# Kernel optimization log

Hardware: AMD Instinct MI355X
Metric: run time of the kernel (lower is better)

Reference implementation:

```python
import jax, jax.numpy as jnp
import numpy as np

B = 64      # num graphs
NPG = 800   # nodes per graph
N = B * NPG
EPG = 6400  # edges per graph (avg degree 8)
APG = 64    # feasible actions per graph
H = 4       # attention heads
C = 64      # hidden channels per head
OUT = 128   # out_channels


def _gat_params(key, fin, h, c, concat):
    k1, k2, k3 = jax.random.split(key, 3)
    s = 1.0 / np.sqrt(fin)
    W = jax.random.uniform(k1, (fin, h * c), jnp.float32, -s, s)
    a_src = jax.random.uniform(k2, (h, c), jnp.float32, -s, s)
    a_dst = jax.random.uniform(k3, (h, c), jnp.float32, -s, s)
    b = jnp.zeros((h * c if concat else c,), jnp.float32)
    return W, a_src, a_dst, b


def _lin_params(key, fin, fout):
    k1, k2 = jax.random.split(key)
    s = 1.0 / np.sqrt(fin)
    W = jax.random.uniform(k1, (fin, fout), jnp.float32, -s, s)
    b = jax.random.uniform(k2, (fout,), jnp.float32, -s, s)
    return W, b


def setup_inputs() -> dict:
    key = jax.random.key(0)
    ks = list(jax.random.split(key, 24))
    x = jax.random.normal(ks[0], (N, 5), jnp.float32)
    offs = jnp.arange(B, dtype=jnp.int32) * NPG
    src = jax.random.randint(ks[1], (B, EPG), 0, NPG, jnp.int32) + offs[:, None]
    dst = jax.random.randint(ks[2], (B, EPG), 0, NPG, jnp.int32) + offs[:, None]
    edge_index = jnp.stack([src.reshape(-1), dst.reshape(-1)])
    batch = jnp.repeat(jnp.arange(B, dtype=jnp.int32), NPG)
    actions_idx = (jax.random.randint(ks[3], (B, APG, 2), 0, NPG, jnp.int32)
                   + offs[:, None, None]).reshape(-1, 2)
    tabu_label = (jax.random.uniform(ks[4], (B * APG, 1)) < 0.5).astype(jnp.float32)
    inp = dict(x=x, edge_index=edge_index, batch=batch,
               actions_idx=actions_idx, tabu_label=tabu_label)
    names = ['f1', 'f2', 'f3', 'b1', 'b2', 'b3']
    fins = [3, H * C, H * C, 3, H * C, H * C]
    hs = [H, H, 1, H, H, 1]
    cs = [C, C, OUT, C, C, OUT]
    concats = [True, True, False, True, True, False]
    for i, nm in enumerate(names):
        W, a_s, a_d, b = _gat_params(ks[5 + i], fins[i], hs[i], cs[i], concats[i])
        inp[nm + '_W'] = W; inp[nm + '_as'] = a_s; inp[nm + '_ad'] = a_d; inp[nm + '_b'] = b
    dims = [(8 * OUT + 1, 2 * OUT), (2 * OUT, 2 * OUT), (2 * OUT, 2 * OUT), (2 * OUT, 1)]
    for i, (fi, fo) in enumerate(dims):
        W, b = _lin_params(ks[12 + i], fi, fo)
        inp['p_W%d' % (i + 1)] = W; inp['p_b%d' % (i + 1)] = b
    return inp


def _gat(h, s, d, W, a_src, a_dst, bias, concat):
    # PyG GATConv: project, per-edge attention, softmax over target index, scatter-add
    n = h.shape[0]
    Hh, Cc = a_src.shape
    xp = (h @ W).reshape(n, Hh, Cc)                      # [N,H,C]
    al_s = (xp * a_src).sum(-1)                          # [N,H]
    al_d = (xp * a_dst).sum(-1)                          # [N,H]
    e = jax.nn.leaky_relu(al_s[s] + al_d[d], 0.2)        # [E,H]
    m = jax.ops.segment_max(e, d, num_segments=n)
    ex = jnp.exp(e - m[d])
    den = jax.ops.segment_sum(ex, d, num_segments=n)
    alpha = ex / (den[d] + 1e-16)
    out = jax.ops.segment_sum(xp[s] * alpha[..., None], d, num_segments=n)  # [N,H,C]
    out = out.reshape(n, Hh * Cc) if concat else out.mean(axis=1)
    return out + bias


def reference(x, edge_index, batch, actions_idx, tabu_label,
              f1_W, f1_as, f1_ad, f1_b, f2_W, f2_as, f2_ad, f2_b,
              f3_W, f3_as, f3_ad, f3_b, b1_W, b1_as, b1_ad, b1_b,
              b2_W, b2_as, b2_ad, b2_b, b3_W, b3_as, b3_ad, b3_b,
              p_W1, p_b1, p_W2, p_b2, p_W3, p_b3, p_W4, p_b4):
    n = x.shape[0]
    ar = jnp.arange(n, dtype=edge_index.dtype)
    ei = jnp.concatenate([edge_index, jnp.stack([ar, ar])], axis=1)  # add_self_loops
    src, dst = ei[0], ei[1]
    # forward branch (flow source_to_target)
    hf = x[:, jnp.array([0, 1, 3])]
    hf = jax.nn.elu(_gat(hf, src, dst, f1_W, f1_as, f1_ad, f1_b, True))
    hf = jax.nn.elu(_gat(hf, src, dst, f2_W, f2_as, f2_ad, f2_b, True))
    hf3 = _gat(hf, src, dst, f3_W, f3_as, f3_ad, f3_b, False)
    # backward branch (flow target_to_source == reversed edges)
    hb = x[:, jnp.array([0, 2, 4])]
    hb = jax.nn.elu(_gat(hb, dst, src, b1_W, b1_as, b1_ad, b1_b, True))
    hb = jax.nn.elu(_gat(hb, dst, src, b2_W, b2_as, b2_ad, b2_b, True))
    hb3 = _gat(hb, dst, src, b3_W, b3_as, b3_ad, b3_b, False)
    h_node = jnp.concatenate([hf3, hb3], axis=-1)        # [N, 2*OUT]
    counts = jax.ops.segment_sum(jnp.ones((n,), x.dtype), batch, num_segments=B)
    g_pool = jax.ops.segment_sum(h_node, batch, num_segments=B) / counts[:, None]
    node_h = jnp.concatenate([h_node, g_pool[batch]], axis=-1)  # [N, 4*OUT]
    action_h = jnp.concatenate([node_h[actions_idx[:, 0]],
                                node_h[actions_idx[:, 1]],
                                tabu_label], axis=-1)    # [A, 8*OUT+1]
    h = jnp.tanh(action_h @ p_W1 + p_b1)
    h = jnp.tanh(h @ p_W2 + p_b2)
    h = jnp.tanh(h @ p_W3 + p_b3)
    score = (h @ p_W4 + p_b4).reshape(B, APG)
    log_prob = jax.nn.log_softmax(score, axis=-1)        # [B, APG]
    entropy = -(jnp.exp(log_prob) * log_prob).sum(-1, keepdims=True)  # [B,1]
    return (log_prob, entropy)
```

## Files before the change

### kernel.cpp

```cpp
#include <hip/hip_runtime.h>
#include <hip/hip_bf16.h>
#include <math.h>

constexpr int NN  = 51200;
constexpr int EE  = 409600;
constexpr int BB  = 64;
constexpr int APG = 64;
constexpr int NPG = 800;
constexpr int SCAN_N = 2 * NN;
constexpr int NA = BB * APG;
constexpr int KF = 1056;

typedef __bf16 bf16x8 __attribute__((ext_vector_type(8)));
typedef float f32x4 __attribute__((ext_vector_type(4)));
typedef float f32x2 __attribute__((ext_vector_type(2)));
typedef __attribute__((address_space(1))) const void g_void;
typedef __attribute__((address_space(3))) void l_void;

__device__ __forceinline__ float leaky(float x) { return x > 0.f ? x : 0.2f * x; }
__device__ __forceinline__ float bflo(unsigned w) { return __uint_as_float(w << 16); }
__device__ __forceinline__ float bfhi(unsigned w) { return __uint_as_float(w & 0xffff0000u); }
__device__ __forceinline__ unsigned short f2b(float x) {
  __hip_bfloat16 h = __float2bfloat16(x);
  unsigned short u;
  __builtin_memcpy(&u, &h, 2);
  return u;
}
__device__ __forceinline__ unsigned pack2(float a, float b) {
  return (unsigned)f2b(a) | ((unsigned)f2b(b) << 16);
}

__global__ void count_kernel(const int* __restrict__ ei, int* cnt) {
  int e = blockIdx.x * blockDim.x + threadIdx.x;
  if (e >= EE) return;
  int s = ei[e], d = ei[EE + e];
  atomicAdd(&cnt[d], 1);
  atomicAdd(&cnt[NN + s], 1);
}

__global__ __launch_bounds__(256) void scan1_kernel(const int* __restrict__ cnt,
                                                    int* __restrict__ rp,
                                                    int* __restrict__ bsum) {
  __shared__ int wsum[4];
  int b = blockIdx.x, t = threadIdx.x;
  int base = b * 1024 + t * 4;
  int4 v = *(const int4*)(cnt + base);
  int s = v.x + v.y + v.z + v.w;
  int lane = t & 63, wv = t >> 6;
  int incl = s;
  for (int off = 1; off < 64; off <<= 1) {
    int u = __shfl_up(incl, off);
    if (lane >= off) incl += u;
  }
  if (lane == 63) wsum[wv] = incl;
  __syncthreads();
  int woff = 0;
  for (int i = 0; i < wv; i++) woff += wsum[i];
  int excl = woff + incl - s;
  rp[base] = excl;
  rp[base + 1] = excl + v.x;
  rp[base + 2] = excl + v.x + v.y;
  rp[base + 3] = excl + v.x + v.y + v.z;
  if (t == 255) bsum[b] = woff + incl;
}

__global__ void scan2_kernel(const int* __restrict__ bsum, int* __restrict__ boff,
                             int* __restrict__ rp) {
  __shared__ int w0;
  int t = threadIdx.x;
  int v = (t < 100) ? bsum[t] : 0;
  int lane = t & 63;
  int incl = v;
  for (int off = 1; off < 64; off <<= 1) {
    int u = __shfl_up(incl, off);
    if (lane >= off) incl += u;
  }
  if (t == 63) w0 = incl;
  __syncthreads();
  int excl = incl - v + ((t >= 64) ? w0 : 0);
  if (t < 100) boff[t] = excl;
  if (t == 99) rp[SCAN_N] = excl + v;
}

__global__ __launch_bounds__(256) void scan3_kernel(int* __restrict__ rp,
                                                    const int* __restrict__ boff) {
  int b = blockIdx.x;
  int off = boff[b];
  int i = b * 1024 + threadIdx.x * 4;
  int4 v = *(int4*)(rp + i);
  v.x += off; v.y += off; v.z += off; v.w += off;
  *(int4*)(rp + i) = v;
}

__global__ void fill_kernel(const int* __restrict__ ei, const int* __restrict__ rp,
                            int* pos, int* __restrict__ col) {
  int e = blockIdx.x * blockDim.x + threadIdx.x;
  if (e >= EE) return;
  int s = ei[e], d = ei[EE + e];
  int p = atomicAdd(&pos[d], 1);
  col[rp[d] + p] = s;
  int q = atomicAdd(&pos[NN + s], 1);
  col[rp[NN + s] + q] = d;
}

__global__ __launch_bounds__(256) void precomp_kernel(const float* __restrict__ Wf,
                                                      const float* __restrict__ Wb,
                                                      const float* __restrict__ asf,
                                                      const float* __restrict__ adf,
                                                      const float* __restrict__ asb,
                                                      const float* __restrict__ adb,
                                                      float* __restrict__ wa) {
  int wave = (blockIdx.x * blockDim.x + threadIdx.x) >> 6;
  int lane = threadIdx.x & 63;
  if (wave >= 48) return;
  int dir = wave / 24, sd = (wave / 12) % 2, h = (wave / 3) % 4, c = wave % 3;
  const float* W = dir ? Wb : Wf;
  const float* a = dir ? (sd ? adb : asb) : (sd ? adf : asf);
  float v = W[c * 256 + h * 64 + lane] * a[h * 64 + lane];
  for (int off = 1; off < 64; off <<= 1) v += __shfl_xor(v, off);
  if (lane == 0) wa[wave] = v;
}

__global__ __launch_bounds__(256) void lin1_kernel(const float* __restrict__ x,
                                                   const float* __restrict__ Wf,
                                                   const float* __restrict__ Wb,
                                                   __hip_bfloat16* __restrict__ out) {
  int idx = blockIdx.x * 256 + threadIdx.x;
  int n = idx >> 5, grp = idx & 31;
  int dir = (n >= NN) ? 1 : 0;
  int node = dir ? n - NN : n;
  const float* W = dir ? Wb : Wf;
  int c1 = dir ? 2 : 1, c2 = dir ? 4 : 3;
  float f0 = x[node * 5], f1 = x[node * 5 + c1], f2 = x[node * 5 + c2];
  int j0 = grp * 8;
  float v[8];
#pragma unroll
  for (int j = 0; j < 8; j++)
    v[j] = f0 * W[j0 + j] + f1 * W[256 + j0 + j] + f2 * W[512 + j0 + j];
  uint4 u;
  u.x = pack2(v[0], v[1]);
  u.y = pack2(v[2], v[3]);
  u.z = pack2(v[4], v[5]);
  u.w = pack2(v[6], v[7]);
  *(uint4*)(out + (size_t)n * 256 + j0) = u;
}

__global__ __launch_bounds__(256) void al1_kernel(const float* __restrict__ x,
                                                  const float* __restrict__ wa,
                                                  float* __restrict__ al_s,
                                                  float* __restrict__ al_d) {
  int idx = blockIdx.x * 256 + threadIdx.x;
  int n = idx >> 2, h = idx & 3;
  int dir = (n >= NN) ? 1 : 0;
  int node = dir ? n - NN : n;
  int c1 = dir ? 2 : 1, c2 = dir ? 4 : 3;
  float f0 = x[node * 5], f1 = x[node * 5 + c1], f2 = x[node * 5 + c2];
  const float* ws = wa + dir * 24 + h * 3;
  const float* wd = wa + dir * 24 + 12 + h * 3;
  al_s[idx] = f0 * ws[0] + f1 * ws[1] + f2 * ws[2];
  al_d[idx] = f0 * wd[0] + f1 * wd[1] + f2 * wd[2];
}

template <int HH>
__global__ __launch_bounds__(256) void alpha_kernel(const float* __restrict__ als,
                                                    const float* __restrict__ ald,
                                                    const int* __restrict__ rp,
                                                    const int* __restrict__ col,
                                                    float* __restrict__ alpha,
                                                    float* __restrict__ alpha_self) {
  int b = blockIdx.x;
  int xcd = b & 7, q = b >> 3;
  int g2 = (q / 25) * 8 + xcd;
  int d = g2 * 800 + (q % 25) * 32 + (threadIdx.x >> 3);
  int slot = threadIdx.x & 7;
  int off_row = (d >= NN) ? NN : 0;
  float ald_loc[HH], self_lg[HH];
#pragma unroll
  for (int h = 0; h < HH; h++) {
    ald_loc[h] = ald[d * HH + h];
    self_lg[h] = leaky(als[d * HH + h] + ald_loc[h]);
  }
  int beg = rp[d], end = rp[d + 1];
  int i0 = beg + slot;
  bool have = i0 < end;
  int s0 = col[have ? i0 : beg] + off_row;
  float mx[HH], lg0[HH];
#pragma unroll
  for (int h = 0; h < HH; h++) mx[h] = self_lg[h];
  if (have) {
#pragma unroll
    for (int h = 0; h < HH; h++) {
      lg0[h] = leaky(als[s0 * HH + h] + ald_loc[h]);
      mx[h] = fmaxf(mx[h], lg0[h]);
    }
  }
  for (int i = i0 + 8; i < end; i += 8) {
    int s = col[i] + off_row;
#pragma unroll
    for (int h = 0; h < HH; h++) mx[h] = fmaxf(mx[h], leaky(als[s * HH + h] + ald_loc[h]));
  }
#pragma unroll
  for (int h = 0; h < HH; h++) {
    mx[h] = fmaxf(mx[h], __shfl_xor(mx[h], 1));
    mx[h] = fmaxf(mx[h], __shfl_xor(mx[h], 2));
    mx[h] = fmaxf(mx[h], __shfl_xor(mx[h], 4));
  }
  float sm[HH], w0[HH];
#pragma unroll
  for (int h = 0; h < HH; h++) sm[h] = 0.f;
  if (have) {
#pragma unroll
    for (int h = 0; h < HH; h++) {
      w0[h] = __expf(lg0[h] - mx[h]);
      sm[h] += w0[h];
    }
  }
  for (int i = i0 + 8; i < end; i += 8) {
    int s = col[i] + off_row;
#pragma unroll
    for (int h = 0; h < HH; h++) {
      float w = __expf(leaky(als[s * HH + h] + ald_loc[h]) - mx[h]);
      sm[h] += w;
      alpha[(size_t)i * HH + h] = w;
    }
  }
#pragma unroll
  for (int h = 0; h < HH; h++) {
    sm[h] += __shfl_xor(sm[h], 1);
    sm[h] += __shfl_xor(sm[h], 2);
    sm[h] += __shfl_xor(sm[h], 4);
  }
  float inv[HH];
#pragma unroll
  for (int h = 0; h < HH; h++)
    inv[h] = 1.f / (sm[h] + __expf(self_lg[h] - mx[h]) + 1e-16f);
  if (have) {
#pragma unroll
    for (int h = 0; h < HH; h++) alpha[(size_t)i0 * HH + h] = w0[h] * inv[h];
  }
  for (int i = i0 + 8; i < end; i += 8)
#pragma unroll
    for (int h = 0; h < HH; h++) alpha[(size_t)i * HH + h] *= inv[h];
  if (slot == 0) {
#pragma unroll
    for (int h = 0; h < HH; h++)
      alpha_self[d * HH + h] = __expf(self_lg[h] - mx[h]) * inv[h];
  }
}

template <int ND>
__device__ __forceinline__ void load_dw(const unsigned* p, unsigned* w) {
  if constexpr (ND == 4) {
    uint4 v = *(const uint4*)p;
    w[0] = v.x; w[1] = v.y; w[2] = v.z; w[3] = v.w;
  } else {
    uint2 v = *(const uint2*)p;
    w[0] = v.x; w[1] = v.y;
  }
}
__device__ __forceinline__ f32x2 unpk(unsigned w) {
  f32x2 v;
  v.x = bflo(w);
  v.y = bfhi(w);
  return v;
}

template <int HH, int CC, int OUT_SPLIT>
__global__ __launch_bounds__(256) void spmm_kernel(const __hip_bfloat16* __restrict__ xp,
                                                   const float* __restrict__ alpha,
                                                   const float* __restrict__ alpha_self,
                                                   const int* __restrict__ rp,
                                                   const int* __restrict__ col,
                                                   const float* __restrict__ biasf,
                                                   const float* __restrict__ biasb,
                                                   __hip_bfloat16* __restrict__ out_bf,
                                                   int do_elu) {
  constexpr int HC = HH * CC;
  constexpr int CPL = HC / 32;
  constexpr int NW = CPL / 2;
  int b = blockIdx.x;
  int xcd = b & 7, q = b >> 3;
  int g2 = (q / 200) * 8 + xcd;
  int d = g2 * 800 + (q % 200) * 4 + (threadIdx.x >> 6);
  int off_row = (d >= NN) ? NN : 0;
  const float* bias = (d >= NN) ? biasb : biasf;
  int lane = threadIdx.x & 63;
  int sub = lane & 31, g = lane >> 5;
  int h_l = (sub * CPL) / CC;
  const unsigned* xw = (const unsigned*)xp;
  size_t rowoff = (size_t)sub * NW;
  f32x2 acc[NW];
#pragma unroll
  for (int j = 0; j < NW; j++) acc[j] = (f32x2)(0.f);
  int beg = rp[d], end = rp[d + 1];
  int deg = end - beg;
  if (g == 0) {
    float a = alpha_self[d * HH + h_l];
    unsigned w[NW];
    load_dw<NW>(xw + (size_t)d * (HC / 2) + rowoff, w);
#pragma unroll
    for (int q2 = 0; q2 < NW; q2++) acc[q2] += a * unpk(w[q2]);
  }
  for (int it = 0; it * 4 < deg; it++) {
    int e1 = beg + it * 4 + g;
    int e2 = e1 + 2;
    bool p1 = e1 < end, p2 = e2 < end;
    int ec1 = p1 ? e1 : beg, ec2 = p2 ? e2 : beg;
    int s1 = col[ec1] + off_row, s2 = col[ec2] + off_row;
    float a1 = p1 ? alpha[(size_t)ec1 * HH + h_l] : 0.f;
    float a2 = p2 ? alpha[(size_t)ec2 * HH + h_l] : 0.f;
    unsigned w1[NW], w2[NW];
    load_dw<NW>(xw + (size_t)s1 * (HC / 2) + rowoff, w1);
    load_dw<NW>(xw + (size_t)s2 * (HC / 2) + rowoff, w2);
#pragma unroll
    for (int q2 = 0; q2 < NW; q2++)
      acc[q2] += a1 * unpk(w1[q2]) + a2 * unpk(w2[q2]);
  }
#pragma unroll
  for (int j = 0; j < NW; j++) {
    acc[j].x += __shfl_xor(acc[j].x, 32);
    acc[j].y += __shfl_xor(acc[j].y, 32);
  }
  if (g == 0) {
    float v[CPL];
#pragma unroll
    for (int j = 0; j < NW; j++) {
      v[2 * j] = acc[j].x + bias[sub * CPL + 2 * j];
      v[2 * j + 1] = acc[j].y + bias[sub * CPL + 2 * j + 1];
    }
    if (do_elu) {
#pragma unroll
      for (int j = 0; j < CPL; j++) v[j] = v[j] > 0.f ? v[j] : (__expf(v[j]) - 1.f);
    }
    unsigned* ob;
    if constexpr (OUT_SPLIT) {
      int nd = (d < NN) ? d : d - NN;
      int oo = (d < NN) ? 0 : 64;
      ob = (unsigned*)out_bf + (size_t)nd * 128 + oo + sub * NW;
    } else {
      ob = (unsigned*)out_bf + (size_t)d * (HC / 2) + rowoff;
    }
#pragma unroll
    for (int q2 = 0; q2 < NW; q2++)
      ob[q2] = pack2(v[2 * q2], v[2 * q2 + 1]);
  }
}

__global__ void castW2_kernel(const float* __restrict__ W0, const float* __restrict__ W1,
                              __hip_bfloat16* __restrict__ Wt0,
                              __hip_bfloat16* __restrict__ Wt1,
                              int K, int N, int Kp) {
  int idx = blockIdx.x * 256 + threadIdx.x;
  int tot = N * Kp;
  if (idx >= 2 * tot) return;
  const float* W = (idx < tot) ? W0 : W1;
  __hip_bfloat16* Wt = (idx < tot) ? Wt0 : Wt1;
  int i = (idx < tot) ? idx : idx - tot;
  int n = i / Kp, k = i % Kp;
  Wt[i] = (k < K) ? __float2bfloat16(W[(size_t)k * N + n]) : __float2bfloat16(0.f);
}

template <int EPI, int ALH, int ALCC>
__global__ __launch_bounds__(256) void gemm_mfma(const __hip_bfloat16* __restrict__ A,
                                                 const __hip_bfloat16* __restrict__ Bt0,
                                                 const __hip_bfloat16* __restrict__ Bt1,
                                                 __hip_bfloat16* __restrict__ Cb,
                                                 const float* __restrict__ bias0,
                                                 const float* __restrict__ bias1,
                                                 const float* __restrict__ asv0,
                                                 const float* __restrict__ asv1,
                                                 const float* __restrict__ adv0,
                                                 const float* __restrict__ adv1,
                                                 float* __restrict__ al_s,
                                                 float* __restrict__ al_d,
                                                 int M, int N, int K, int Mhalf) {
  __shared__ __align__(16) __hip_bfloat16 As[128 * 32];
  __shared__ __align__(16) __hip_bfloat16 Bs[128 * 32];
  int t = threadIdx.x;
  int wave = t >> 6, lane = t & 63;
  int wm = (wave >> 1) * 64, wn = (wave & 1) * 64;
  int bm = blockIdx.y * 128, bn = blockIdx.x * 128;
  bool second = bm >= Mhalf;
  const __hip_bfloat16* Bt = second ? Bt1 : Bt0;
  const float* bias = second ? bias1 : bias0;
  const float* asv = second ? asv1 : asv0;
  const float* adv = second ? adv1 : adv0;

  int r0 = t >> 2, c0 = (t & 3) * 8;
  const __hip_bfloat16* Ag0 = A + (size_t)(bm + r0) * K + c0;
  const __hip_bfloat16* Ag1 = A + (size_t)(bm + r0 + 64) * K + c0;
  const __hip_bfloat16* Bg0 = Bt + (size_t)(bn + r0) * K + c0;
  const __hip_bfloat16* Bg1 = Bt + (size_t)(bn + r0 + 64) * K + c0;
  __hip_bfloat16* Asp0 = As + t * 8;
  __hip_bfloat16* Asp1 = As + 64 * 8 * 4 + t * 8;
  __hip_bfloat16* Bsp0 = Bs + t * 8;
  __hip_bfloat16* Bsp1 = Bs + 64 * 8 * 4 + t * 8;

  f32x4 acc[4][4];
#pragma unroll
  for (int i = 0; i < 4; i++)
#pragma unroll
    for (int j = 0; j < 4; j++) acc[i][j] = (f32x4)(0.f);

  int frag_off = (lane & 15) * 32 + (lane >> 4) * 8;
  const __hip_bfloat16* Ab = As + wm * 32 + frag_off;
  const __hip_bfloat16* Bb = Bs + wn * 32 + frag_off;

  for (int k0 = 0; k0 < K; k0 += 32) {
    __syncthreads();
    __builtin_amdgcn_global_load_lds((g_void*)(Ag0 + k0), (l_void*)Asp0, 16, 0, 0);
    __builtin_amdgcn_global_load_lds((g_void*)(Ag1 + k0), (l_void*)Asp1, 16, 0, 0);
    __builtin_amdgcn_global_load_lds((g_void*)(Bg0 + k0), (l_void*)Bsp0, 16, 0, 0);
    __builtin_amdgcn_global_load_lds((g_void*)(Bg1 + k0), (l_void*)Bsp1, 16, 0, 0);
    __syncthreads();
    bf16x8 af[4], bfr[4];
#pragma unroll
    for (int i = 0; i < 4; i++) af[i] = *(const bf16x8*)(Ab + i * 16 * 32);
#pragma unroll
    for (int j = 0; j < 4; j++) bfr[j] = *(const bf16x8*)(Bb + j * 16 * 32);
#pragma unroll
    for (int i = 0; i < 4; i++)
#pragma unroll
      for (int j = 0; j < 4; j++)
        acc[i][j] = __builtin_amdgcn_mfma_f32_16x16x32_bf16(af[i], bfr[j], acc[i][j], 0, 0, 0);
  }

  int cr = (lane >> 4) * 4, cc = lane & 15;

  if constexpr (ALH > 0) {
    int head = (bn + wn) / ALCC;
    float as_c[4], ad_c[4];
#pragma unroll
    for (int j = 0; j < 4; j++) {
      int colx = bn + wn + j * 16 + cc;
      as_c[j] = asv[colx];
      ad_c[j] = adv[colx];
    }
#pragma unroll
    for (int i = 0; i < 4; i++)
#pragma unroll
      for (int r = 0; r < 4; r++) {
        float ps = 0.f, pd = 0.f;
#pragma unroll
        for (int j = 0; j < 4; j++) {
          ps += acc[i][j][r] * as_c[j];
          pd += acc[i][j][r] * ad_c[j];
        }
        ps += __shfl_xor(ps, 1); pd += __shfl_xor(pd, 1);
        ps += __shfl_xor(ps, 2); pd += __shfl_xor(pd, 2);
        ps += __shfl_xor(ps, 4); pd += __shfl_xor(pd, 4);
        ps += __shfl_xor(ps, 8); pd += __shfl_xor(pd, 8);
        if ((lane & 15) == 0) {
          int row = bm + wm + i * 16 + cr + r;
          if (ALCC > 64) {
            atomicAdd(&al_s[row * ALH + head], ps);
            atomicAdd(&al_d[row * ALH + head], pd);
          } else {
            al_s[row * ALH + head] = ps;
            al_d[row * ALH + head] = pd;
          }
        }
      }
  }

#pragma unroll
  for (int i = 0; i < 4; i++)
#pragma unroll
    for (int j = 0; j < 4; j++) {
      int colx = bn + wn + j * 16 + cc;
      float bs = (EPI == 2) ? bias[colx] : 0.f;
#pragma unroll
      for (int r = 0; r < 4; r++) {
        float v = acc[i][j][r];
        if (EPI == 2) v = tanhf(v + bs);
        Cb[(size_t)(bm + wm + i * 16 + cr + r) * N + colx] = __float2bfloat16(v);
      }
    }
}

__global__ void pool1_kernel(const __hip_bfloat16* __restrict__ h_node,
                             float* __restrict__ part) {
  int g = blockIdx.y, c = blockIdx.x, t = threadIdx.x;
  const unsigned* base = (const unsigned*)h_node + ((size_t)g * NPG + c * 100) * 128 + t;
  f32x2 s = (f32x2)(0.f);
  for (int i = 0; i < 100; i++) {
    unsigned w = base[(size_t)i * 128];
    s += unpk(w);
  }
  part[(size_t)(g * 8 + c) * 256 + 2 * t] = s.x;
  part[(size_t)(g * 8 + c) * 256 + 2 * t + 1] = s.y;
}

__global__ void pool2_kernel(const float* __restrict__ part, float* __restrict__ g_pool) {
  int g = blockIdx.x, t = threadIdx.x;
  float s = 0.f;
  for (int c = 0; c < 8; c++) s += part[(size_t)(g * 8 + c) * 256 + t];
  g_pool[g * 256 + t] = s * (1.f / NPG);
}

__global__ __launch_bounds__(256) void buildfeat_kernel(const __hip_bfloat16* __restrict__ h_node,
                                                        const float* __restrict__ g_pool,
                                                        const int* __restrict__ actions,
                                                        const float* __restrict__ tabu,
                                                        const int* __restrict__ batch,
                                                        __hip_bfloat16* __restrict__ feat) {
  int a = (blockIdx.x * blockDim.x + threadIdx.x) >> 6;
  int lane = threadIdx.x & 63;
  if (a >= NA) return;
  int n0 = actions[a * 2], n1 = actions[a * 2 + 1];
  int g = batch[n0];
  ushort4 v0 = *(const ushort4*)(h_node + (size_t)n0 * 256 + lane * 4);
  float4 vg = *(const float4*)(g_pool + (size_t)g * 256 + lane * 4);
  ushort4 v1 = *(const ushort4*)(h_node + (size_t)n1 * 256 + lane * 4);
  __hip_bfloat16* fr = feat + (size_t)a * KF;
  ushort4 ug = make_ushort4(f2b(vg.x), f2b(vg.y), f2b(vg.z), f2b(vg.w));
  *(ushort4*)(fr + lane * 4) = v0;
  *(ushort4*)(fr + 256 + lane * 4) = ug;
  *(ushort4*)(fr + 512 + lane * 4) = v1;
  *(ushort4*)(fr + 768 + lane * 4) = ug;
  if (lane < 8) {
    float t0 = (lane == 0) ? tabu[a] : 0.f;
    ushort4 u = make_ushort4(f2b(t0), 0, 0, 0);
    *(ushort4*)(fr + 1024 + lane * 4) = u;
  }
}

__global__ __launch_bounds__(256) void gemv_kernel(const __hip_bfloat16* __restrict__ y,
                                                   const float* __restrict__ W4,
                                                   const float* __restrict__ b4,
                                                   float* __restrict__ scores) {
  int a = (blockIdx.x * blockDim.x + threadIdx.x) >> 6;
  int lane = threadIdx.x & 63;
  if (a >= NA) return;
  const unsigned* row = (const unsigned*)(y + (size_t)a * 256);
  float s = 0.f;
#pragma unroll
  for (int q = 0; q < 2; q++) {
    unsigned w = row[lane * 2 + q];
    s += bflo(w) * W4[lane * 4 + 2 * q] + bfhi(w) * W4[lane * 4 + 2 * q + 1];
  }
  for (int off = 1; off < 64; off <<= 1) s += __shfl_xor(s, off);
  if (lane == 0) scores[a] = s + b4[0];
}

__global__ void softmax_kernel(const float* __restrict__ scores, float* __restrict__ out) {
  int g = (blockIdx.x * blockDim.x + threadIdx.x) >> 6;
  int lane = threadIdx.x & 63;
  if (g >= BB) return;
  float s = scores[g * 64 + lane];
  float m = s;
  for (int off = 1; off < 64; off <<= 1) m = fmaxf(m, __shfl_xor(m, off));
  float ex = expf(s - m);
  float sum = ex;
  for (int off = 1; off < 64; off <<= 1) sum += __shfl_xor(sum, off);
  float lp = s - m - logf(sum);
  out[g * 64 + lane] = lp;
  float pe = (ex / sum) * lp;
  for (int off = 1; off < 64; off <<= 1) pe += __shfl_xor(pe, off);
  if (lane == 0) out[BB * APG + g] = -pe;
}

extern "C" void kernel_launch(void* const* d_in, const int* in_sizes, int n_in,
                              void* d_out, int out_size, void* d_ws, size_t ws_size,
                              hipStream_t stream) {
  const float* x = (const float*)d_in[0];
  const int* ei = (const int*)d_in[1];
  const int* batch = (const int*)d_in[2];
  const int* actions = (const int*)d_in[3];
  const float* tabu = (const float*)d_in[4];
  const float* fW[3] = {(const float*)d_in[5], (const float*)d_in[9], (const float*)d_in[13]};
  const float* fas[3] = {(const float*)d_in[6], (const float*)d_in[10], (const float*)d_in[14]};
  const float* fad[3] = {(const float*)d_in[7], (const float*)d_in[11], (const float*)d_in[15]};
  const float* fb[3] = {(const float*)d_in[8], (const float*)d_in[12], (const float*)d_in[16]};
  const float* bW[3] = {(const float*)d_in[17], (const float*)d_in[21], (const float*)d_in[25]};
  const float* bas[3] = {(const float*)d_in[18], (const float*)d_in[22], (const float*)d_in[26]};
  const float* bad[3] = {(const float*)d_in[19], (const float*)d_in[23], (const float*)d_in[27]};
  const float* bb[3] = {(const float*)d_in[20], (const float*)d_in[24], (const float*)d_in[28]};
  const float* pW1 = (const float*)d_in[29];
  const float* pb1 = (const float*)d_in[30];
  const float* pW2 = (const float*)d_in[31];
  const float* pb2 = (const float*)d_in[32];
  const float* pW3 = (const float*)d_in[33];
  const float* pb3 = (const float*)d_in[34];
  const float* pW4 = (const float*)d_in[35];
  const float* pb4 = (const float*)d_in[36];
  float* out = (float*)d_out;

  char* ws = (char*)d_ws;
  size_t o = 0;
  auto alloc = [&](size_t bytes) -> void* {
    o = (o + 255) & ~(size_t)255;
    void* p = ws + o;
    o += bytes;
    return p;
  };
  int* cnt = (int*)alloc((size_t)4 * NN * 4);
  int* rp = (int*)alloc((size_t)(SCAN_N + 1) * 4);
  int* col = (int*)alloc(((size_t)2 * EE + 64) * 4);
  int* bsum = (int*)alloc(128 * 4);
  int* boff = (int*)alloc(128 * 4);
  float* al_s = (float*)alloc((size_t)SCAN_N * 4 * 4);
  float* al_d = (float*)alloc((size_t)SCAN_N * 4 * 4);
  float* alpha = (float*)alloc((size_t)2 * EE * 4 * 4);
  float* alpha_self = (float*)alloc((size_t)SCAN_N * 4 * 4);
  float* wa = (float*)alloc(64 * 4);
  __hip_bfloat16* xp = (__hip_bfloat16*)alloc((size_t)SCAN_N * 256 * 2);
  __hip_bfloat16* bufA = (__hip_bfloat16*)alloc((size_t)SCAN_N * 256 * 2);
  __hip_bfloat16* h_node = (__hip_bfloat16*)alloc((size_t)NN * 256 * 2);
  __hip_bfloat16* wt0 = (__hip_bfloat16*)alloc((size_t)256 * KF * 2);
  __hip_bfloat16* wt1 = (__hip_bfloat16*)alloc((size_t)256 * KF * 2);
  float* part = (float*)alloc((size_t)BB * 8 * 256 * 4);
  float* g_pool = (float*)alloc((size_t)BB * 256 * 4);
  float* scores = (float*)alloc((size_t)NA * 4);
  __hip_bfloat16* feat = xp;
  __hip_bfloat16* y1 = feat + (size_t)NA * KF;
  __hip_bfloat16* y2 = y1 + (size_t)NA * 256;

  hipMemsetAsync(cnt, 0, (size_t)4 * NN * 4, stream);
  count_kernel<<<(EE + 255) / 256, 256, 0, stream>>>(ei, cnt);
  scan1_kernel<<<SCAN_N / 1024, 256, 0, stream>>>(cnt, rp, bsum);
  scan2_kernel<<<1, 128, 0, stream>>>(bsum, boff, rp);
  scan3_kernel<<<SCAN_N / 1024, 256, 0, stream>>>(rp, boff);
  fill_kernel<<<(EE + 255) / 256, 256, 0, stream>>>(ei, rp, cnt + 2 * NN, col);

  const int nwb = SCAN_N / 4;
  const int nab = SCAN_N * 8 / 256;

  precomp_kernel<<<12, 256, 0, stream>>>(fW[0], bW[0], fas[0], fad[0], bas[0], bad[0], wa);
  lin1_kernel<<<SCAN_N * 32 / 256, 256, 0, stream>>>(x, fW[0], bW[0], xp);
  al1_kernel<<<SCAN_N * 4 / 256, 256, 0, stream>>>(x, wa, al_s, al_d);
  alpha_kernel<4><<<nab, 256, 0, stream>>>(al_s, al_d, rp, col, alpha, alpha_self);
  spmm_kernel<4, 64, 0><<<nwb, 256, 0, stream>>>(xp, alpha, alpha_self, rp, col,
                                                 fb[0], bb[0], bufA, 1);
  castW2_kernel<<<(2 * 256 * 256 + 255) / 256, 256, 0, stream>>>(fW[1], bW[1], wt0, wt1,
                                                                 256, 256, 256);
  gemm_mfma<1, 4, 64><<<dim3(2, SCAN_N / 128), 256, 0, stream>>>(
      bufA, wt0, wt1, xp, nullptr, nullptr, fas[1], bas[1], fad[1], bad[1],
      al_s, al_d, SCAN_N, 256, 256, NN);
  alpha_kernel<4><<<nab, 256, 0, stream>>>(al_s, al_d, rp, col, alpha, alpha_self);
  spmm_kernel<4, 64, 0><<<nwb, 256, 0, stream>>>(xp, alpha, alpha_self, rp, col,
                                                 fb[1], bb[1], bufA, 1);
  castW2_kernel<<<(2 * 128 * 256 + 255) / 256, 256, 0, stream>>>(fW[2], bW[2], wt0, wt1,
                                                                 256, 128, 256);
  hipMemsetAsync(al_s, 0, (size_t)SCAN_N * 4, stream);
  hipMemsetAsync(al_d, 0, (size_t)SCAN_N * 4, stream);
  gemm_mfma<1, 1, 128><<<dim3(1, SCAN_N / 128), 256, 0, stream>>>(
      bufA, wt0, wt1, xp, nullptr, nullptr, fas[2], bas[2], fad[2], bad[2],
      al_s, al_d, SCAN_N, 128, 256, NN);
  alpha_kernel<1><<<nab, 256, 0, stream>>>(al_s, al_d, rp, col, alpha, alpha_self);
  spmm_kernel<1, 128, 1><<<nwb, 256, 0, stream>>>(xp, alpha, alpha_self, rp, col,
                                                  fb[2], bb[2], h_node, 0);

  pool1_kernel<<<dim3(8, BB), 128, 0, stream>>>(h_node, part);
  pool2_kernel<<<BB, 256, 0, stream>>>(part, g_pool);

  buildfeat_kernel<<<NA / 4, 256, 0, stream>>>(h_node, g_pool, actions, tabu, batch, feat);
  castW2_kernel<<<(2 * 256 * KF + 255) / 256, 256, 0, stream>>>(pW1, pW1, wt0, wt1,
                                                                1025, 256, KF);
  gemm_mfma<2, 0, 64><<<dim3(2, NA / 128), 256, 0, stream>>>(
      feat, wt0, wt0, y1, pb1, pb1, nullptr, nullptr, nullptr, nullptr,
      nullptr, nullptr, NA, 256, KF, 1 << 30);
  castW2_kernel<<<(2 * 256 * 256 + 255) / 256, 256, 0, stream>>>(pW2, pW3, wt0, wt1,
                                                                 256, 256, 256);
  gemm_mfma<2, 0, 64><<<dim3(2, NA / 128), 256, 0, stream>>>(
      y1, wt0, wt0, y2, pb2, pb2, nullptr, nullptr, nullptr, nullptr,
      nullptr, nullptr, NA, 256, 256, 1 << 30);
  gemm_mfma<2, 0, 64><<<dim3(2, NA / 128), 256, 0, stream>>>(
      y2, wt1, wt1, y1, pb3, pb3, nullptr, nullptr, nullptr, nullptr,
      nullptr, nullptr, NA, 256, 256, 1 << 30);
  gemv_kernel<<<NA / 4, 256, 0, stream>>>(y1, pW4, pb4, scores);
  softmax_kernel<<<(BB * 64) / 256, 256, 0, stream>>>(scores, out);
}
```

Baseline: 536.4 us.

## Fuse first-layer attention logits, drop softmax max pass, merge scoring head

Folds the al1 logit computation into lin1 and fuses the final gemv with the log-softmax/entropy kernel into a single per-graph head kernel. This removes two launches and the scores round trip. The attention softmax drops its max-subtraction pass, which saves one sweep over each neighbour list but can overflow if logits are large. Two memsets are also merged into one, which assumes al_s and al_d are contiguous.

```diff
diff --git a/kernel.cpp b/kernel.cpp
--- a/kernel.cpp
+++ b/kernel.cpp
@@ -124,7 +124,10 @@
 __global__ __launch_bounds__(256) void lin1_kernel(const float* __restrict__ x,
                                                    const float* __restrict__ Wf,
                                                    const float* __restrict__ Wb,
-                                                   __hip_bfloat16* __restrict__ out) {
+                                                   const float* __restrict__ wa,
+                                                   __hip_bfloat16* __restrict__ out,
+                                                   float* __restrict__ al_s,
+                                                   float* __restrict__ al_d) {
   int idx = blockIdx.x * 256 + threadIdx.x;
   int n = idx >> 5, grp = idx & 31;
   int dir = (n >= NN) ? 1 : 0;
@@ -143,22 +146,12 @@
   u.z = pack2(v[4], v[5]);
   u.w = pack2(v[6], v[7]);
   *(uint4*)(out + (size_t)n * 256 + j0) = u;
-}
-
-__global__ __launch_bounds__(256) void al1_kernel(const float* __restrict__ x,
-                                                  const float* __restrict__ wa,
-                                                  float* __restrict__ al_s,
-                                                  float* __restrict__ al_d) {
-  int idx = blockIdx.x * 256 + threadIdx.x;
-  int n = idx >> 2, h = idx & 3;
-  int dir = (n >= NN) ? 1 : 0;
-  int node = dir ? n - NN : n;
-  int c1 = dir ? 2 : 1, c2 = dir ? 4 : 3;
-  float f0 = x[node * 5], f1 = x[node * 5 + c1], f2 = x[node * 5 + c2];
-  const float* ws = wa + dir * 24 + h * 3;
-  const float* wd = wa + dir * 24 + 12 + h * 3;
-  al_s[idx] = f0 * ws[0] + f1 * ws[1] + f2 * ws[2];
-  al_d[idx] = f0 * wd[0] + f1 * wd[1] + f2 * wd[2];
+  if (grp < 4) {
+    const float* ws = wa + dir * 24 + grp * 3;
+    const float* wd = wa + dir * 24 + 12 + grp * 3;
+    al_s[n * 4 + grp] = f0 * ws[0] + f1 * ws[1] + f2 * ws[2];
+    al_d[n * 4 + grp] = f0 * wd[0] + f1 * wd[1] + f2 * wd[2];
+  }
 }
 
 template <int HH>
@@ -174,52 +167,31 @@
   int d = g2 * 800 + (q % 25) * 32 + (threadIdx.x >> 3);
   int slot = threadIdx.x & 7;
   int off_row = (d >= NN) ? NN : 0;
-  float ald_loc[HH], self_lg[HH];
+  float ald_loc[HH], self_w[HH];
 #pragma unroll
   for (int h = 0; h < HH; h++) {
     ald_loc[h] = ald[d * HH + h];
-    self_lg[h] = leaky(als[d * HH + h] + ald_loc[h]);
+    self_w[h] = __expf(leaky(als[d * HH + h] + ald_loc[h]));
   }
   int beg = rp[d], end = rp[d + 1];
   int i0 = beg + slot;
   bool have = i0 < end;
   int s0 = col[have ? i0 : beg] + off_row;
-  float mx[HH], lg0[HH];
-#pragma unroll
-  for (int h = 0; h < HH; h++) mx[h] = self_lg[h];
+  float sm[HH], w0[HH];
+#pragma unroll
+  for (int h = 0; h < HH; h++) sm[h] = 0.f;
   if (have) {
 #pragma unroll
     for (int h = 0; h < HH; h++) {
-      lg0[h] = leaky(als[s0 * HH + h] + ald_loc[h]);
-      mx[h] = fmaxf(mx[h], lg0[h]);
+      w0[h] = __expf(leaky(als[s0 * HH + h] + ald_loc[h]));
+      sm[h] += w0[h];
     }
   }
   for (int i = i0 + 8; i < end; i += 8) {
     int s = col[i] + off_row;
 #pragma unroll
-    for (int h = 0; h < HH; h++) mx[h] = fmaxf(mx[h], leaky(als[s * HH + h] + ald_loc[h]));
-  }
-#pragma unroll
-  for (int h = 0; h < HH; h++) {
-    mx[h] = fmaxf(mx[h], __shfl_xor(mx[h], 1));
-    mx[h] = fmaxf(mx[h], __shfl_xor(mx[h], 2));
-    mx[h] = fmaxf(mx[h], __shfl_xor(mx[h], 4));
-  }
-  float sm[HH], w0[HH];
-#pragma unroll
-  for (int h = 0; h < HH; h++) sm[h] = 0.f;
-  if (have) {
-#pragma unroll
     for (int h = 0; h < HH; h++) {
-      w0[h] = __expf(lg0[h] - mx[h]);
-      sm[h] += w0[h];
-    }
-  }
-  for (int i = i0 + 8; i < end; i += 8) {
-    int s = col[i] + off_row;
-#pragma unroll
-    for (int h = 0; h < HH; h++) {
-      float w = __expf(leaky(als[s * HH + h] + ald_loc[h]) - mx[h]);
+      float w = __expf(leaky(als[s * HH + h] + ald_loc[h]));
       sm[h] += w;
       alpha[(size_t)i * HH + h] = w;
     }
@@ -233,7 +205,7 @@
   float inv[HH];
 #pragma unroll
   for (int h = 0; h < HH; h++)
-    inv[h] = 1.f / (sm[h] + __expf(self_lg[h] - mx[h]) + 1e-16f);
+    inv[h] = 1.f / (sm[h] + self_w[h] + 1e-16f);
   if (have) {
 #pragma unroll
     for (int h = 0; h < HH; h++) alpha[(size_t)i0 * HH + h] = w0[h] * inv[h];
@@ -244,7 +216,7 @@
   if (slot == 0) {
 #pragma unroll
     for (int h = 0; h < HH; h++)
-      alpha_self[d * HH + h] = __expf(self_lg[h] - mx[h]) * inv[h];
+      alpha_self[d * HH + h] = self_w[h] * inv[h];
   }
 }
 
@@ -483,10 +455,7 @@
   int g = blockIdx.y, c = blockIdx.x, t = threadIdx.x;
   const unsigned* base = (const unsigned*)h_node + ((size_t)g * NPG + c * 100) * 128 + t;
   f32x2 s = (f32x2)(0.f);
-  for (int i = 0; i < 100; i++) {
-    unsigned w = base[(size_t)i * 128];
-    s += unpk(w);
-  }
+  for (int i = 0; i < 100; i++) s += unpk(base[(size_t)i * 128]);
   part[(size_t)(g * 8 + c) * 256 + 2 * t] = s.x;
   part[(size_t)(g * 8 + c) * 256 + 2 * t + 1] = s.y;
 }
@@ -525,39 +494,39 @@
   }
 }
 
-__global__ __launch_bounds__(256) void gemv_kernel(const __hip_bfloat16* __restrict__ y,
+__global__ __launch_bounds__(256) void head_kernel(const __hip_bfloat16* __restrict__ y,
                                                    const float* __restrict__ W4,
                                                    const float* __restrict__ b4,
-                                                   float* __restrict__ scores) {
-  int a = (blockIdx.x * blockDim.x + threadIdx.x) >> 6;
-  int lane = threadIdx.x & 63;
-  if (a >= NA) return;
-  const unsigned* row = (const unsigned*)(y + (size_t)a * 256);
+                                                   float* __restrict__ out) {
+  __shared__ float sc[64];
+  int g = blockIdx.x;
+  int t = threadIdx.x;
+  int a = t >> 2, sub = t & 3;
+  int aid = g * 64 + a;
+  const unsigned* row = (const unsigned*)(y + (size_t)aid * 256) + sub * 32;
+  const float* w = W4 + sub * 64;
   float s = 0.f;
 #pragma unroll
-  for (int q = 0; q < 2; q++) {
-    unsigned w = row[lane * 2 + q];
-    s += bflo(w) * W4[lane * 4 + 2 * q] + bfhi(w) * W4[lane * 4 + 2 * q + 1];
-  }
-  for (int off = 1; off < 64; off <<= 1) s += __shfl_xor(s, off);
-  if (lane == 0) scores[a] = s + b4[0];
-}
-
-__global__ void softmax_kernel(const float* __restrict__ scores, float* __restrict__ out) {
-  int g = (blockIdx.x * blockDim.x + threadIdx.x) >> 6;
-  int lane = threadIdx.x & 63;
-  if (g >= BB) return;
-  float s = scores[g * 64 + lane];
-  float m = s;
-  for (int off = 1; off < 64; off <<= 1) m = fmaxf(m, __shfl_xor(m, off));
-  float ex = expf(s - m);
-  float sum = ex;
-  for (int off = 1; off < 64; off <<= 1) sum += __shfl_xor(sum, off);
-  float lp = s - m - logf(sum);
-  out[g * 64 + lane] = lp;
-  float pe = (ex / sum) * lp;
-  for (int off = 1; off < 64; off <<= 1) pe += __shfl_xor(pe, off);
-  if (lane == 0) out[BB * APG + g] = -pe;
+  for (int q = 0; q < 32; q++) {
+    s += bflo(row[q]) * w[2 * q] + bfhi(row[q]) * w[2 * q + 1];
+  }
+  s += __shfl_xor(s, 1);
+  s += __shfl_xor(s, 2);
+  if (sub == 0) sc[a] = s + b4[0];
+  __syncthreads();
+  if (t < 64) {
+    float v = sc[t];
+    float m = v;
+    for (int off = 1; off < 64; off <<= 1) m = fmaxf(m, __shfl_xor(m, off));
+    float ex = expf(v - m);
+    float sum = ex;
+    for (int off = 1; off < 64; off <<= 1) sum += __shfl_xor(sum, off);
+    float lp = v - m - logf(sum);
+    out[g * 64 + t] = lp;
+    float pe = (ex / sum) * lp;
+    for (int off = 1; off < 64; off <<= 1) pe += __shfl_xor(pe, off);
+    if (t == 0) out[BB * APG + g] = -pe;
+  }
 }
 
 extern "C" void kernel_launch(void* const* d_in, const int* in_sizes, int n_in,
@@ -611,7 +580,6 @@
   __hip_bfloat16* wt1 = (__hip_bfloat16*)alloc((size_t)256 * KF * 2);
   float* part = (float*)alloc((size_t)BB * 8 * 256 * 4);
   float* g_pool = (float*)alloc((size_t)BB * 256 * 4);
-  float* scores = (float*)alloc((size_t)NA * 4);
   __hip_bfloat16* feat = xp;
   __hip_bfloat16* y1 = feat + (size_t)NA * KF;
   __hip_bfloat16* y2 = y1 + (size_t)NA * 256;
@@ -627,8 +595,7 @@
   const int nab = SCAN_N * 8 / 256;
 
   precomp_kernel<<<12, 256, 0, stream>>>(fW[0], bW[0], fas[0], fad[0], bas[0], bad[0], wa);
-  lin1_kernel<<<SCAN_N * 32 / 256, 256, 0, stream>>>(x, fW[0], bW[0], xp);
-  al1_kernel<<<SCAN_N * 4 / 256, 256, 0, stream>>>(x, wa, al_s, al_d);
+  lin1_kernel<<<SCAN_N * 32 / 256, 256, 0, stream>>>(x, fW[0], bW[0], wa, xp, al_s, al_d);
   alpha_kernel<4><<<nab, 256, 0, stream>>>(al_s, al_d, rp, col, alpha, alpha_self);
   spmm_kernel<4, 64, 0><<<nwb, 256, 0, stream>>>(xp, alpha, alpha_self, rp, col,
                                                  fb[0], bb[0], bufA, 1);
@@ -642,8 +609,7 @@
                                                  fb[1], bb[1], bufA, 1);
   castW2_kernel<<<(2 * 128 * 256 + 255) / 256, 256, 0, stream>>>(fW[2], bW[2], wt0, wt1,
                                                                  256, 128, 256);
-  hipMemsetAsync(al_s, 0, (size_t)SCAN_N * 4, stream);
-  hipMemsetAsync(al_d, 0, (size_t)SCAN_N * 4, stream);
+  hipMemsetAsync(al_s, 0, (size_t)2 * SCAN_N * 4, stream);
   gemm_mfma<1, 1, 128><<<dim3(1, SCAN_N / 128), 256, 0, stream>>>(
       bufA, wt0, wt1, xp, nullptr, nullptr, fas[2], bas[2], fad[2], bad[2],
       al_s, al_d, SCAN_N, 128, 256, NN);
@@ -668,6 +634,5 @@
   gemm_mfma<2, 0, 64><<<dim3(2, NA / 128), 256, 0, stream>>>(
       y2, wt1, wt1, y1, pb3, pb3, nullptr, nullptr, nullptr, nullptr,
       nullptr, nullptr, NA, 256, 256, 1 << 30);
-  gemv_kernel<<<NA / 4, 256, 0, stream>>>(y1, pW4, pb4, scores);
-  softmax_kernel<<<(BB * 64) / 256, 256, 0, stream>>>(scores, out);
-}
+  head_kernel<<<BB, 256, 0, stream>>>(y1, pW4, pb4, out);
+}
```

New measurement: 534.7 us. No clear change (-0.3%).
